# Kernel optimization log

Measured on AMD Instinct MI355X. Metric: run time of the kernel, lower is better.

The kernel has to match this reference:

```python
import jax, jax.numpy as jnp
import numpy as np

HEADS = 12
D_MODEL = 768
D_K = D_MODEL // HEADS


def setup_inputs() -> dict:
    key = jax.random.key(0)
    ks = jax.random.split(key, 5)
    B, S = 2, 2048
    scale = 1.0 / np.sqrt(D_MODEL)
    return {
        "q": jax.random.normal(ks[0], (B, S, D_MODEL), dtype=jnp.float32),
        "k": jax.random.normal(ks[1], (B, S, D_MODEL), dtype=jnp.float32),
        "v": jax.random.normal(ks[2], (B, S, D_MODEL), dtype=jnp.float32),
        "Wk": jax.random.normal(ks[3], (D_MODEL, D_MODEL), dtype=jnp.float32) * scale,
        "bk": jnp.zeros((D_MODEL,), dtype=jnp.float32),
        "Wo": jax.random.normal(ks[4], (D_MODEL, D_MODEL), dtype=jnp.float32) * scale,
        "bo": jnp.zeros((D_MODEL,), dtype=jnp.float32),
    }


def reference(q, k, v, Wk, bk, Wo, bo):
    B, S, _ = q.shape
    # NOTE: faithful to source bug: q, k, v ALL projected with k_linear.
    def proj(x):
        y = x @ Wk.T + bk                    # [B,S,D]
        return y.reshape(B, -1, HEADS, D_K).transpose(0, 2, 1, 3)  # [B,H,S,Dk]

    qh, kh, vh = proj(q), proj(k), proj(v)
    scores = jnp.einsum('bhsd,bhtd->bhst', qh, kh) / jnp.sqrt(jnp.float32(D_K))
    attn = jax.nn.softmax(scores, axis=-1)   # dropout is identity in eval
    out = jnp.einsum('bhst,bhtd->bhsd', attn, vh)
    concat = out.transpose(0, 2, 1, 3).reshape(B, -1, D_MODEL)
    return concat @ Wo.T + bo
```

## Files before the change

### kernel.cpp

```cpp
#include <hip/hip_runtime.h>
#include <hip/hip_bf16.h>
#include <stddef.h>

#define HEADS 12
#define DM 768
#define DK 64
#define SEQ 2048
#define NB 2
#define WSZ (DM * DM)

typedef __attribute__((ext_vector_type(8))) short short8;
typedef __attribute__((ext_vector_type(4))) float f32x4;

#define MFMA16(A, B, C) __builtin_amdgcn_mfma_f32_16x16x32_bf16((A), (B), (C), 0, 0, 0)

__device__ __forceinline__ unsigned short f2bf(float x) {
  union { float f; unsigned u; } c;
  c.f = x;
  unsigned r = (c.u + 0x7FFFu + ((c.u >> 16) & 1u)) >> 16;
  return (unsigned short)r;
}
__device__ __forceinline__ float bf2f(unsigned short h) {
  union { float f; unsigned u; } c;
  c.u = ((unsigned)h) << 16;
  return c.f;
}

__device__ __forceinline__ void async16(const void* g, void* l) {
  __builtin_amdgcn_global_load_lds(
      (const __attribute__((address_space(1))) void*)g,
      (__attribute__((address_space(3))) void*)l, 16, 0, 0);
}

__device__ __forceinline__ void splitpk(float a, float b, unsigned& hu, unsigned& lu) {
  union { __hip_bfloat162 v; unsigned u; } c;
  c.v = __float22bfloat162_rn(make_float2(a, b));
  hu = c.u;
  const float ra = a - bf2f((unsigned short)(hu & 0xFFFFu));
  const float rb = b - bf2f((unsigned short)(hu >> 16));
  c.v = __float22bfloat162_rn(make_float2(ra, rb));
  lu = c.u;
}

__device__ __forceinline__ unsigned pk2bf(float a, float b) {
  union { __hip_bfloat162 v; unsigned u; } c;
  c.v = __float22bfloat162_rn(make_float2(a, b));
  return c.u;
}

__global__ __launch_bounds__(256) void split_w(const float* __restrict__ S,
                                               unsigned short* __restrict__ H,
                                               unsigned short* __restrict__ L,
                                               int n) {
  const int i = (blockIdx.x * 256 + threadIdx.x) * 8;
  if (i >= n) return;
  float a[8];
  *(float4*)&a[0] = *(const float4*)&S[i];
  *(float4*)&a[4] = *(const float4*)&S[i + 4];
  unsigned hu[4], lu[4];
#pragma unroll
  for (int u = 0; u < 4; ++u) splitpk(a[2 * u], a[2 * u + 1], hu[u], lu[u]);
  *(uint4*)&H[i] = *(uint4*)&hu[0];
  *(uint4*)&L[i] = *(uint4*)&lu[0];
}

__global__ __launch_bounds__(256) void split_qkv(
    const float* __restrict__ Q, const float* __restrict__ K,
    const float* __restrict__ V, unsigned short* __restrict__ QH,
    unsigned short* __restrict__ QL, unsigned short* __restrict__ KH,
    unsigned short* __restrict__ VH) {
  const int y = blockIdx.y;
  const float* __restrict__ S = (y == 0) ? Q : (y == 1) ? K : V;
  const int i = (blockIdx.x * 256 + threadIdx.x) * 8;
  float a[8];
  *(float4*)&a[0] = *(const float4*)&S[i];
  *(float4*)&a[4] = *(const float4*)&S[i + 4];
  if (y == 0) {
    unsigned hu[4], lu[4];
#pragma unroll
    for (int u = 0; u < 4; ++u) splitpk(a[2 * u], a[2 * u + 1], hu[u], lu[u]);
    *(uint4*)&QH[i] = *(uint4*)&hu[0];
    *(uint4*)&QL[i] = *(uint4*)&lu[0];
  } else {
    unsigned hu[4];
#pragma unroll
    for (int u = 0; u < 4; ++u) hu[u] = pk2bf(a[2 * u], a[2 * u + 1]);
    unsigned short* __restrict__ D = (y == 1) ? KH : VH;
    *(uint4*)&D[i] = *(uint4*)&hu[0];
  }
}

__global__ __launch_bounds__(256, 3) void gemm_proj(
    const unsigned short* __restrict__ Xh_, const unsigned short* __restrict__ Xl_,
    const unsigned short* __restrict__ Kh_, const unsigned short* __restrict__ Vh_,
    const unsigned short* __restrict__ Bh_, const unsigned short* __restrict__ Bl_,
    const float* __restrict__ bias, unsigned short* __restrict__ q_h,
    unsigned short* __restrict__ q_l, unsigned short* __restrict__ k_h,
    unsigned short* __restrict__ vt_h) {
  __shared__ __align__(16) short Ash[128 * 32];
  __shared__ __align__(16) short Asl[128 * 32];
  __shared__ __align__(16) short Bsh[96 * 32];
  __shared__ __align__(16) short Bsl[96 * 32];

  const int tid = threadIdx.x;
  const int z = blockIdx.z;
  const unsigned short* __restrict__ Ah = (z == 0) ? Xh_ : (z == 1) ? Kh_ : Vh_;
  const int id = blockIdx.x;
  const int m0 = (id & 31) << 7, n0 = (id >> 5) * 96;
  const int lane = tid & 63, wv = tid >> 6;
  const int l15 = lane & 15, quad = lane >> 4;
  const int wm = (wv >> 1) * 64, wn = (wv & 1) * 48;
  const int c0 = wv * 64 + lane, c1 = 256 + c0;
  const int b0 = (wv * 64) << 3, b1 = (256 + wv * 64) << 3;

  f32x4 acc[4][3];
#pragma unroll
  for (int i = 0; i < 4; ++i)
#pragma unroll
    for (int j = 0; j < 3; ++j) acc[i][j] = (f32x4){0.f, 0.f, 0.f, 0.f};

  for (int k0 = 0; k0 < DM; k0 += 32) {
    __syncthreads();
    async16(&Ah[(size_t)(m0 + (c0 >> 2)) * DM + k0 + (c0 & 3) * 8], &Ash[b0]);
    async16(&Ah[(size_t)(m0 + (c1 >> 2)) * DM + k0 + (c1 & 3) * 8], &Ash[b1]);
    if (z == 0) {
      async16(&Xl_[(size_t)(m0 + (c0 >> 2)) * DM + k0 + (c0 & 3) * 8], &Asl[b0]);
      async16(&Xl_[(size_t)(m0 + (c1 >> 2)) * DM + k0 + (c1 & 3) * 8], &Asl[b1]);
    }
    async16(&Bh_[(size_t)(n0 + (c0 >> 2)) * DM + k0 + (c0 & 3) * 8], &Bsh[b0]);
    async16(&Bl_[(size_t)(n0 + (c0 >> 2)) * DM + k0 + (c0 & 3) * 8], &Bsl[b0]);
    if (wv < 2) {
      async16(&Bh_[(size_t)(n0 + (c1 >> 2)) * DM + k0 + (c1 & 3) * 8], &Bsh[b1]);
      async16(&Bl_[(size_t)(n0 + (c1 >> 2)) * DM + k0 + (c1 & 3) * 8], &Bsl[b1]);
    }
    __syncthreads();

    short8 bh8[3], bl8[3];
#pragma unroll
    for (int nt = 0; nt < 3; ++nt) {
      bh8[nt] = *(const short8*)&Bsh[(wn + nt * 16 + l15) * 32 + quad * 8];
      bl8[nt] = *(const short8*)&Bsl[(wn + nt * 16 + l15) * 32 + quad * 8];
    }
#pragma unroll
    for (int mt = 0; mt < 4; ++mt) {
      const short8 ah8 = *(const short8*)&Ash[(wm + mt * 16 + l15) * 32 + quad * 8];
#pragma unroll
      for (int nt = 0; nt < 3; ++nt) {
        acc[mt][nt] = MFMA16(ah8, bh8[nt], acc[mt][nt]);
        acc[mt][nt] = MFMA16(ah8, bl8[nt], acc[mt][nt]);
      }
      if (z == 0) {
        const short8 al8 = *(const short8*)&Asl[(wm + mt * 16 + l15) * 32 + quad * 8];
#pragma unroll
        for (int nt = 0; nt < 3; ++nt) acc[mt][nt] = MFMA16(al8, bh8[nt], acc[mt][nt]);
      }
    }
  }

#pragma unroll
  for (int mt = 0; mt < 4; ++mt)
#pragma unroll
    for (int nt = 0; nt < 3; ++nt) {
      const int n = n0 + wn + nt * 16 + l15;
      const float bv = bias[n];
      const int hh = n >> 6, dk = n & 63;
#pragma unroll
      for (int j = 0; j < 4; ++j) {
        const int m = m0 + wm + mt * 16 + quad * 4 + j;
        const float y = acc[mt][nt][j] + bv;
        const int b = m >> 11, s = m & 2047;
        const unsigned short yh = f2bf(y);
        if (z == 0) {
          const int a = ((b * HEADS + hh) * SEQ + s) * DK + dk;
          q_h[a] = yh;
          q_l[a] = f2bf(y - bf2f(yh));
        } else if (z == 1) {
          k_h[((b * HEADS + hh) * SEQ + s) * DK + dk] = yh;
        } else {
          vt_h[((b * HEADS + hh) * DK + dk) * SEQ + s] = yh;
        }
      }
    }
}

__global__ __launch_bounds__(256, 2) void gemm_out(
    const unsigned short* __restrict__ Ah_, const unsigned short* __restrict__ Al_,
    const unsigned short* __restrict__ Bh_, const unsigned short* __restrict__ Bl_,
    const float* __restrict__ bias, float* __restrict__ outF) {
  __shared__ __align__(16) short Ash[64 * 32];
  __shared__ __align__(16) short Asl[64 * 32];
  __shared__ __align__(16) short Bsh[96 * 32];
  __shared__ __align__(16) short Bsl[96 * 32];

  const int tid = threadIdx.x;
  const int id = blockIdx.x;
  const int m0 = (id & 63) << 6, n0 = (id >> 6) * 96;
  const int lane = tid & 63, wv = tid >> 6;
  const int l15 = lane & 15, quad = lane >> 4;
  const int wm = (wv >> 1) * 32, wn = (wv & 1) * 48;
  const int c0 = wv * 64 + lane, c1 = 256 + c0;
  const int b0 = (wv * 64) << 3, b1 = (256 + wv * 64) << 3;

  f32x4 acc[2][3];
#pragma unroll
  for (int i = 0; i < 2; ++i)
#pragma unroll
    for (int j = 0; j < 3; ++j) acc[i][j] = (f32x4){0.f, 0.f, 0.f, 0.f};

  for (int k0 = 0; k0 < DM; k0 += 32) {
    __syncthreads();
    async16(&Ah_[(size_t)(m0 + (c0 >> 2)) * DM + k0 + (c0 & 3) * 8], &Ash[b0]);
    async16(&Al_[(size_t)(m0 + (c0 >> 2)) * DM + k0 + (c0 & 3) * 8], &Asl[b0]);
    async16(&Bh_[(size_t)(n0 + (c0 >> 2)) * DM + k0 + (c0 & 3) * 8], &Bsh[b0]);
    async16(&Bl_[(size_t)(n0 + (c0 >> 2)) * DM + k0 + (c0 & 3) * 8], &Bsl[b0]);
    if (wv < 2) {
      async16(&Bh_[(size_t)(n0 + (c1 >> 2)) * DM + k0 + (c1 & 3) * 8], &Bsh[b1]);
      async16(&Bl_[(size_t)(n0 + (c1 >> 2)) * DM + k0 + (c1 & 3) * 8], &Bsl[b1]);
    }
    __syncthreads();

    short8 bh8[3], bl8[3];
#pragma unroll
    for (int nt = 0; nt < 3; ++nt) {
      bh8[nt] = *(const short8*)&Bsh[(wn + nt * 16 + l15) * 32 + quad * 8];
      bl8[nt] = *(const short8*)&Bsl[(wn + nt * 16 + l15) * 32 + quad * 8];
    }
#pragma unroll
    for (int mt = 0; mt < 2; ++mt) {
      const short8 ah8 = *(const short8*)&Ash[(wm + mt * 16 + l15) * 32 + quad * 8];
      const short8 al8 = *(const short8*)&Asl[(wm + mt * 16 + l15) * 32 + quad * 8];
#pragma unroll
      for (int nt = 0; nt < 3; ++nt) {
        acc[mt][nt] = MFMA16(ah8, bh8[nt], acc[mt][nt]);
        acc[mt][nt] = MFMA16(al8, bh8[nt], acc[mt][nt]);
        acc[mt][nt] = MFMA16(ah8, bl8[nt], acc[mt][nt]);
      }
    }
  }

#pragma unroll
  for (int mt = 0; mt < 2; ++mt)
#pragma unroll
    for (int nt = 0; nt < 3; ++nt) {
      const int n = n0 + wn + nt * 16 + l15;
      const float bv = bias[n];
#pragma unroll
      for (int j = 0; j < 4; ++j) {
        const int m = m0 + wm + mt * 16 + quad * 4 + j;
        outF[(size_t)m * DM + n] = acc[mt][nt][j] + bv;
      }
    }
}

__global__ __launch_bounds__(256, 3) void attn_mfma(
    const unsigned short* __restrict__ q_h, const unsigned short* __restrict__ q_l,
    const unsigned short* __restrict__ k_h, const unsigned short* __restrict__ vt_h,
    unsigned short* __restrict__ cch, unsigned short* __restrict__ ccl) {
  __shared__ __align__(16) short Ks[2][64 * 32];
  __shared__ __align__(16) short Vs[2][64 * 32];
  __shared__ __align__(16) short Ps[4][16 * 72];
  __shared__ float Lred[4][16];

  const int tid = threadIdx.x, lane = tid & 63, wv = tid >> 6;
  const int l15 = lane & 15, quad = lane >> 4;
  const int id = blockIdx.x;
  const int bh = id % 24, q0 = (id / 24) << 6;
  const int qw = q0 + (wv << 4);
  const int crow = (wv * 64 + lane) >> 2, csub = (lane & 3) * 8;
  const int ldsb = (wv * 64) << 3;

  short8 Qf[2][2];
#pragma unroll
  for (int ks = 0; ks < 2; ++ks) {
    const int off = (bh * SEQ + qw + l15) * DK + ks * 32 + quad * 8;
    Qf[ks][0] = *(const short8*)&q_h[off];
    Qf[ks][1] = *(const short8*)&q_l[off];
  }

  f32x4 O[4];
#pragma unroll
  for (int j = 0; j < 4; ++j) O[j] = (f32x4){0.f, 0.f, 0.f, 0.f};
  float lsum = 0.f;

  const int kbase = bh * SEQ * DK;
  const int vbase = bh * DK * SEQ;

  for (int t0 = 0; t0 < SEQ; t0 += 64) {
    __syncthreads();
    async16(&k_h[kbase + (t0 + crow) * DK + csub], &Ks[0][ldsb]);
    async16(&k_h[kbase + (t0 + crow) * DK + 32 + csub], &Ks[1][ldsb]);
    async16(&vt_h[vbase + crow * SEQ + t0 + csub], &Vs[0][ldsb]);
    async16(&vt_h[vbase + crow * SEQ + t0 + 32 + csub], &Vs[1][ldsb]);
    __syncthreads();

    f32x4 St[4];
#pragma unroll
    for (int tt = 0; tt < 4; ++tt) St[tt] = (f32x4){0.f, 0.f, 0.f, 0.f};
#pragma unroll
    for (int ks = 0; ks < 2; ++ks)
#pragma unroll
      for (int tt = 0; tt < 4; ++tt) {
        const short8 kh8 = *(const short8*)&Ks[ks][(tt * 16 + l15) * 32 + quad * 8];
        St[tt] = MFMA16(kh8, Qf[ks][0], St[tt]);
        St[tt] = MFMA16(kh8, Qf[ks][1], St[tt]);
      }

#pragma unroll
    for (int tt = 0; tt < 4; ++tt) {
      const float p0 = __expf(fminf(St[tt][0] * 0.125f, 30.f));
      const float p1 = __expf(fminf(St[tt][1] * 0.125f, 30.f));
      const float p2 = __expf(fminf(St[tt][2] * 0.125f, 30.f));
      const float p3 = __expf(fminf(St[tt][3] * 0.125f, 30.f));
      lsum += (p0 + p1) + (p2 + p3);
      unsigned pk[2];
      pk[0] = pk2bf(p0, p1);
      pk[1] = pk2bf(p2, p3);
      *(uint2*)&Ps[wv][l15 * 72 + tt * 16 + quad * 4] = *(uint2*)&pk[0];
    }
    asm volatile("s_waitcnt lgkmcnt(0)" ::: "memory");

#pragma unroll
    for (int ks = 0; ks < 2; ++ks) {
      const short8 pf = *(const short8*)&Ps[wv][l15 * 72 + ks * 32 + quad * 8];
#pragma unroll
      for (int nt = 0; nt < 4; ++nt) {
        const short8 vh8 = *(const short8*)&Vs[ks][(nt * 16 + l15) * 32 + quad * 8];
        O[nt] = MFMA16(pf, vh8, O[nt]);
      }
    }
  }

  float ls = lsum;
  ls += __shfl_xor(ls, 16);
  ls += __shfl_xor(ls, 32);
  if (quad == 0) Lred[wv][l15] = ls;
  asm volatile("s_waitcnt lgkmcnt(0)" ::: "memory");
  __builtin_amdgcn_wave_barrier();

  const int b = bh / HEADS, hh = bh % HEADS;
#pragma unroll
  for (int j = 0; j < 4; ++j) {
    const float invj = 1.0f / Lred[wv][quad * 4 + j];
    const int qrow = q0 + (wv << 4) + quad * 4 + j;
#pragma unroll
    for (int nt = 0; nt < 4; ++nt) {
      const float y = O[nt][j] * invj;
      const size_t a = ((size_t)b * SEQ + qrow) * DM + hh * DK + nt * 16 + l15;
      const unsigned short yh = f2bf(y);
      cch[a] = yh;
      ccl[a] = f2bf(y - bf2f(yh));
    }
  }
}

extern "C" void kernel_launch(void* const* d_in, const int* in_sizes, int n_in,
                              void* d_out, int out_size, void* d_ws,
                              size_t ws_size, hipStream_t stream) {
  const float* q = (const float*)d_in[0];
  const float* k = (const float*)d_in[1];
  const float* v = (const float*)d_in[2];
  const float* Wk = (const float*)d_in[3];
  const float* bk = (const float*)d_in[4];
  const float* Wo = (const float*)d_in[5];
  const float* bo = (const float*)d_in[6];
  float* out = (float*)d_out;

  const size_t SZ = (size_t)NB * SEQ * DM;
  unsigned short* ws16 = (unsigned short*)d_ws;
  unsigned short* xq_h = ws16;
  unsigned short* xq_l = ws16 + SZ;
  unsigned short* xk_h = ws16 + 2 * SZ;
  unsigned short* xv_h = ws16 + 3 * SZ;
  unsigned short* cch = xq_h;
  unsigned short* ccl = xq_l;
  unsigned short* woh = xk_h;
  unsigned short* wol = xk_h + WSZ;
  unsigned short* qp_h = ws16 + 4 * SZ;
  unsigned short* qp_l = ws16 + 5 * SZ;
  unsigned short* kp_h = ws16 + 6 * SZ;
  unsigned short* vtp_h = ws16 + 7 * SZ;
  unsigned short* wkh = ws16 + 8 * SZ;
  unsigned short* wkl = wkh + WSZ;

  split_qkv<<<dim3(SZ / 2048, 3), 256, 0, stream>>>(q, k, v, xq_h, xq_l, xk_h,
                                                    xv_h);
  split_w<<<dim3(WSZ / 2048), 256, 0, stream>>>(Wk, wkh, wkl, WSZ);
  gemm_proj<<<dim3(256, 1, 3), 256, 0, stream>>>(xq_h, xq_l, xk_h, xv_h, wkh,
                                                 wkl, bk, qp_h, qp_l, kp_h,
                                                 vtp_h);
  attn_mfma<<<dim3(768), 256, 0, stream>>>(qp_h, qp_l, kp_h, vtp_h, cch, ccl);
  split_w<<<dim3(WSZ / 2048), 256, 0, stream>>>(Wo, woh, wol, WSZ);
  gemm_out<<<dim3(512), 256, 0, stream>>>(cch, ccl, woh, wol, bo, out);
}
```

Measured before the change: 217.7 us.

## Merge split kernels into one launch and re-tile attention waves as 2x2 split-K

The three preprocessing launches (q/k/v split, Wk split, Wo split) become a single prep_split kernel, so two launches disappear and Wo gets its own workspace region. The attention kernel changes each wave from 16 query rows over all 64 keys to 32 query rows over half of each 64-key tile. Each loaded K fragment now feeds two query tiles, and each V fragment feeds two output tiles. The two key-halves are combined at the end through a shared-memory reduction of O and the row sums. This trades more registers and an extra LDS buffer plus two block barriers for fewer LDS reads per MFMA.

```diff
diff --git a/kernel.cpp b/kernel.cpp
--- a/kernel.cpp
+++ b/kernel.cpp
@@ -48,45 +48,39 @@
   return c.u;
 }
 
-__global__ __launch_bounds__(256) void split_w(const float* __restrict__ S,
-                                               unsigned short* __restrict__ H,
-                                               unsigned short* __restrict__ L,
-                                               int n) {
-  const int i = (blockIdx.x * 256 + threadIdx.x) * 8;
-  if (i >= n) return;
+__global__ __launch_bounds__(256) void prep_split(
+    const float* __restrict__ q, const float* __restrict__ k,
+    const float* __restrict__ v, const float* __restrict__ Wk,
+    const float* __restrict__ Wo, unsigned short* __restrict__ xq_h,
+    unsigned short* __restrict__ xq_l, unsigned short* __restrict__ xk_h,
+    unsigned short* __restrict__ xv_h, unsigned short* __restrict__ wkh,
+    unsigned short* __restrict__ wkl, unsigned short* __restrict__ woh,
+    unsigned short* __restrict__ wol) {
+  const int id = blockIdx.x;
+  const float* S;
+  unsigned short *H, *L = nullptr;
+  int base;
+  if (id < 1536) { S = q; H = xq_h; L = xq_l; base = id; }
+  else if (id < 3072) { S = k; H = xk_h; base = id - 1536; }
+  else if (id < 4608) { S = v; H = xv_h; base = id - 3072; }
+  else if (id < 4896) { S = Wk; H = wkh; L = wkl; base = id - 4608; }
+  else { S = Wo; H = woh; L = wol; base = id - 4896; }
+
+  const int i = (base * 256 + threadIdx.x) * 8;
   float a[8];
   *(float4*)&a[0] = *(const float4*)&S[i];
   *(float4*)&a[4] = *(const float4*)&S[i + 4];
-  unsigned hu[4], lu[4];
-#pragma unroll
-  for (int u = 0; u < 4; ++u) splitpk(a[2 * u], a[2 * u + 1], hu[u], lu[u]);
-  *(uint4*)&H[i] = *(uint4*)&hu[0];
-  *(uint4*)&L[i] = *(uint4*)&lu[0];
-}
-
-__global__ __launch_bounds__(256) void split_qkv(
-    const float* __restrict__ Q, const float* __restrict__ K,
-    const float* __restrict__ V, unsigned short* __restrict__ QH,
-    unsigned short* __restrict__ QL, unsigned short* __restrict__ KH,
-    unsigned short* __restrict__ VH) {
-  const int y = blockIdx.y;
-  const float* __restrict__ S = (y == 0) ? Q : (y == 1) ? K : V;
-  const int i = (blockIdx.x * 256 + threadIdx.x) * 8;
-  float a[8];
-  *(float4*)&a[0] = *(const float4*)&S[i];
-  *(float4*)&a[4] = *(const float4*)&S[i + 4];
-  if (y == 0) {
+  if (L) {
     unsigned hu[4], lu[4];
 #pragma unroll
     for (int u = 0; u < 4; ++u) splitpk(a[2 * u], a[2 * u + 1], hu[u], lu[u]);
-    *(uint4*)&QH[i] = *(uint4*)&hu[0];
-    *(uint4*)&QL[i] = *(uint4*)&lu[0];
+    *(uint4*)&H[i] = *(uint4*)&hu[0];
+    *(uint4*)&L[i] = *(uint4*)&lu[0];
   } else {
     unsigned hu[4];
 #pragma unroll
     for (int u = 0; u < 4; ++u) hu[u] = pk2bf(a[2 * u], a[2 * u + 1]);
-    unsigned short* __restrict__ D = (y == 1) ? KH : VH;
-    *(uint4*)&D[i] = *(uint4*)&hu[0];
+    *(uint4*)&H[i] = *(uint4*)&hu[0];
   }
 }
 
@@ -258,29 +252,35 @@
     unsigned short* __restrict__ cch, unsigned short* __restrict__ ccl) {
   __shared__ __align__(16) short Ks[2][64 * 32];
   __shared__ __align__(16) short Vs[2][64 * 32];
-  __shared__ __align__(16) short Ps[4][16 * 72];
-  __shared__ float Lred[4][16];
+  __shared__ __align__(16) short Ps[4][32 * 40];
+  __shared__ float Osh[64 * 68];
+  __shared__ float Lred[4][2][16];
 
   const int tid = threadIdx.x, lane = tid & 63, wv = tid >> 6;
   const int l15 = lane & 15, quad = lane >> 4;
+  const int qh = wv & 1, th = wv >> 1;
   const int id = blockIdx.x;
   const int bh = id % 24, q0 = (id / 24) << 6;
-  const int qw = q0 + (wv << 4);
   const int crow = (wv * 64 + lane) >> 2, csub = (lane & 3) * 8;
   const int ldsb = (wv * 64) << 3;
 
-  short8 Qf[2][2];
-#pragma unroll
-  for (int ks = 0; ks < 2; ++ks) {
-    const int off = (bh * SEQ + qw + l15) * DK + ks * 32 + quad * 8;
-    Qf[ks][0] = *(const short8*)&q_h[off];
-    Qf[ks][1] = *(const short8*)&q_l[off];
-  }
-
-  f32x4 O[4];
-#pragma unroll
-  for (int j = 0; j < 4; ++j) O[j] = (f32x4){0.f, 0.f, 0.f, 0.f};
-  float lsum = 0.f;
+  short8 Qf[2][2][2];
+#pragma unroll
+  for (int qt = 0; qt < 2; ++qt)
+#pragma unroll
+    for (int ks = 0; ks < 2; ++ks) {
+      const int off =
+          (bh * SEQ + q0 + qh * 32 + qt * 16 + l15) * DK + ks * 32 + quad * 8;
+      Qf[qt][ks][0] = *(const short8*)&q_h[off];
+      Qf[qt][ks][1] = *(const short8*)&q_l[off];
+    }
+
+  f32x4 O[2][4];
+#pragma unroll
+  for (int i = 0; i < 2; ++i)
+#pragma unroll
+    for (int j = 0; j < 4; ++j) O[i][j] = (f32x4){0.f, 0.f, 0.f, 0.f};
+  float lsum[2] = {0.f, 0.f};
 
   const int kbase = bh * SEQ * DK;
   const int vbase = bh * DK * SEQ;
@@ -293,63 +293,94 @@
     async16(&vt_h[vbase + crow * SEQ + t0 + 32 + csub], &Vs[1][ldsb]);
     __syncthreads();
 
-    f32x4 St[4];
-#pragma unroll
-    for (int tt = 0; tt < 4; ++tt) St[tt] = (f32x4){0.f, 0.f, 0.f, 0.f};
+    f32x4 St[2][2];
+#pragma unroll
+    for (int i = 0; i < 2; ++i)
+#pragma unroll
+      for (int j = 0; j < 2; ++j) St[i][j] = (f32x4){0.f, 0.f, 0.f, 0.f};
 #pragma unroll
     for (int ks = 0; ks < 2; ++ks)
 #pragma unroll
-      for (int tt = 0; tt < 4; ++tt) {
-        const short8 kh8 = *(const short8*)&Ks[ks][(tt * 16 + l15) * 32 + quad * 8];
-        St[tt] = MFMA16(kh8, Qf[ks][0], St[tt]);
-        St[tt] = MFMA16(kh8, Qf[ks][1], St[tt]);
-      }
-
-#pragma unroll
-    for (int tt = 0; tt < 4; ++tt) {
-      const float p0 = __expf(fminf(St[tt][0] * 0.125f, 30.f));
-      const float p1 = __expf(fminf(St[tt][1] * 0.125f, 30.f));
-      const float p2 = __expf(fminf(St[tt][2] * 0.125f, 30.f));
-      const float p3 = __expf(fminf(St[tt][3] * 0.125f, 30.f));
-      lsum += (p0 + p1) + (p2 + p3);
-      unsigned pk[2];
-      pk[0] = pk2bf(p0, p1);
-      pk[1] = pk2bf(p2, p3);
-      *(uint2*)&Ps[wv][l15 * 72 + tt * 16 + quad * 4] = *(uint2*)&pk[0];
-    }
+      for (int tt = 0; tt < 2; ++tt) {
+        const short8 kh8 =
+            *(const short8*)&Ks[ks][(th * 32 + tt * 16 + l15) * 32 + quad * 8];
+#pragma unroll
+        for (int qt = 0; qt < 2; ++qt) {
+          St[tt][qt] = MFMA16(kh8, Qf[qt][ks][0], St[tt][qt]);
+          St[tt][qt] = MFMA16(kh8, Qf[qt][ks][1], St[tt][qt]);
+        }
+      }
+
+#pragma unroll
+    for (int tt = 0; tt < 2; ++tt)
+#pragma unroll
+      for (int qt = 0; qt < 2; ++qt) {
+        const float p0 = __expf(fminf(St[tt][qt][0] * 0.125f, 30.f));
+        const float p1 = __expf(fminf(St[tt][qt][1] * 0.125f, 30.f));
+        const float p2 = __expf(fminf(St[tt][qt][2] * 0.125f, 30.f));
+        const float p3 = __expf(fminf(St[tt][qt][3] * 0.125f, 30.f));
+        lsum[qt] += (p0 + p1) + (p2 + p3);
+        unsigned pk[2];
+        pk[0] = pk2bf(p0, p1);
+        pk[1] = pk2bf(p2, p3);
+        *(uint2*)&Ps[wv][(qt * 16 + l15) * 40 + tt * 16 + quad * 4] =
+            *(uint2*)&pk[0];
+      }
     asm volatile("s_waitcnt lgkmcnt(0)" ::: "memory");
 
-#pragma unroll
-    for (int ks = 0; ks < 2; ++ks) {
-      const short8 pf = *(const short8*)&Ps[wv][l15 * 72 + ks * 32 + quad * 8];
-#pragma unroll
-      for (int nt = 0; nt < 4; ++nt) {
-        const short8 vh8 = *(const short8*)&Vs[ks][(nt * 16 + l15) * 32 + quad * 8];
-        O[nt] = MFMA16(pf, vh8, O[nt]);
-      }
-    }
-  }
-
-  float ls = lsum;
-  ls += __shfl_xor(ls, 16);
-  ls += __shfl_xor(ls, 32);
-  if (quad == 0) Lred[wv][l15] = ls;
-  asm volatile("s_waitcnt lgkmcnt(0)" ::: "memory");
-  __builtin_amdgcn_wave_barrier();
-
-  const int b = bh / HEADS, hh = bh % HEADS;
-#pragma unroll
-  for (int j = 0; j < 4; ++j) {
-    const float invj = 1.0f / Lred[wv][quad * 4 + j];
-    const int qrow = q0 + (wv << 4) + quad * 4 + j;
+    short8 pf[2];
+#pragma unroll
+    for (int qt = 0; qt < 2; ++qt)
+      pf[qt] = *(const short8*)&Ps[wv][(qt * 16 + l15) * 40 + quad * 8];
 #pragma unroll
     for (int nt = 0; nt < 4; ++nt) {
-      const float y = O[nt][j] * invj;
-      const size_t a = ((size_t)b * SEQ + qrow) * DM + hh * DK + nt * 16 + l15;
-      const unsigned short yh = f2bf(y);
-      cch[a] = yh;
-      ccl[a] = f2bf(y - bf2f(yh));
-    }
+      const short8 vh8 =
+          *(const short8*)&Vs[th][(nt * 16 + l15) * 32 + quad * 8];
+      O[0][nt] = MFMA16(pf[0], vh8, O[0][nt]);
+      O[1][nt] = MFMA16(pf[1], vh8, O[1][nt]);
+    }
+  }
+
+#pragma unroll
+  for (int qt = 0; qt < 2; ++qt) {
+    float l = lsum[qt];
+    l += __shfl_xor(l, 16);
+    l += __shfl_xor(l, 32);
+    if (quad == 0) Lred[wv][qt][l15] = l;
+  }
+  __syncthreads();
+  if (th == 1) {
+#pragma unroll
+    for (int qt = 0; qt < 2; ++qt)
+#pragma unroll
+      for (int nt = 0; nt < 4; ++nt)
+#pragma unroll
+        for (int j = 0; j < 4; ++j)
+          Osh[(qh * 32 + qt * 16 + quad * 4 + j) * 68 + nt * 16 + l15] =
+              O[qt][nt][j];
+  }
+  __syncthreads();
+  if (th == 0) {
+    const int b = bh / HEADS, hh = bh % HEADS;
+#pragma unroll
+    for (int qt = 0; qt < 2; ++qt)
+#pragma unroll
+      for (int j = 0; j < 4; ++j) {
+        const int qloc = qt * 16 + quad * 4 + j;
+        const float inv =
+            1.0f / (Lred[wv][qt][quad * 4 + j] + Lred[wv + 2][qt][quad * 4 + j]);
+        const int qrow = q0 + qh * 32 + qloc;
+#pragma unroll
+        for (int nt = 0; nt < 4; ++nt) {
+          const float y =
+              (O[qt][nt][j] + Osh[(qh * 32 + qloc) * 68 + nt * 16 + l15]) * inv;
+          const size_t a =
+              ((size_t)b * SEQ + qrow) * DM + hh * DK + nt * 16 + l15;
+          const unsigned short yh = f2bf(y);
+          cch[a] = yh;
+          ccl[a] = f2bf(y - bf2f(yh));
+        }
+      }
   }
 }
 
@@ -373,22 +404,20 @@
   unsigned short* xv_h = ws16 + 3 * SZ;
   unsigned short* cch = xq_h;
   unsigned short* ccl = xq_l;
-  unsigned short* woh = xk_h;
-  unsigned short* wol = xk_h + WSZ;
   unsigned short* qp_h = ws16 + 4 * SZ;
   unsigned short* qp_l = ws16 + 5 * SZ;
   unsigned short* kp_h = ws16 + 6 * SZ;
   unsigned short* vtp_h = ws16 + 7 * SZ;
   unsigned short* wkh = ws16 + 8 * SZ;
   unsigned short* wkl = wkh + WSZ;
-
-  split_qkv<<<dim3(SZ / 2048, 3), 256, 0, stream>>>(q, k, v, xq_h, xq_l, xk_h,
-                                                    xv_h);
-  split_w<<<dim3(WSZ / 2048), 256, 0, stream>>>(Wk, wkh, wkl, WSZ);
+  unsigned short* woh = wkl + WSZ;
+  unsigned short* wol = woh + WSZ;
+
+  prep_split<<<dim3(5184), 256, 0, stream>>>(q, k, v, Wk, Wo, xq_h, xq_l, xk_h,
+                                             xv_h, wkh, wkl, woh, wol);
   gemm_proj<<<dim3(256, 1, 3), 256, 0, stream>>>(xq_h, xq_l, xk_h, xv_h, wkh,
                                                  wkl, bk, qp_h, qp_l, kp_h,
                                                  vtp_h);
   attn_mfma<<<dim3(768), 256, 0, stream>>>(qp_h, qp_l, kp_h, vtp_h, cch, ccl);
-  split_w<<<dim3(WSZ / 2048), 256, 0, stream>>>(Wo, woh, wol, WSZ);
   gemm_out<<<dim3(512), 256, 0, stream>>>(cch, ccl, woh, wol, bo, out);
 }
```

After: 209.2 us. 1.04x faster.
